# Kernel optimization log

Hardware: AMD Instinct MI355X
Metric: run time of the kernel (lower is better)

The kernel has to match this reference:

```python
import jax, jax.numpy as jnp
import numpy as np

EMBED_DIM = 768
NUM_HEADS = 8
HEAD_DIM = EMBED_DIM // NUM_HEADS
WINDOW_HALF = (17 - 1) // 2          # window_size=17 -> 8
GAP = 3 + 1                          # dilation_gap=3 -> stride 4
OVERLAP = WINDOW_HALF * GAP          # 32
N_LINES = 8192


def setup_inputs() -> dict:
    key = jax.random.key(0)
    k1, k2, k3, k4, k5 = jax.random.split(key, 5)
    D = EMBED_DIM
    return {
        "main": jax.random.normal(k1, (N_LINES, D), dtype=jnp.float32),
        "begin": jax.random.normal(k2, (OVERLAP, D), dtype=jnp.float32),
        "end": jax.random.normal(k3, (OVERLAP, D), dtype=jnp.float32),
        "in_proj_w": jax.random.normal(k4, (3 * D, D), dtype=jnp.float32) * 0.02,
        "in_proj_b": jnp.zeros((3 * D,), dtype=jnp.float32),
        "out_proj_w": jax.random.normal(k5, (D, D), dtype=jnp.float32) * 0.02,
        "out_proj_b": jnp.zeros((D,), dtype=jnp.float32),
    }


def reference(main, begin, end, in_proj_w, in_proj_b, out_proj_w, out_proj_b):
    N, D = main.shape
    H, hd = NUM_HEADS, HEAD_DIM
    # combined buffer [begin | main | end]; the per-token shifted concatenations
    # in the torch loop are equivalent to a strided gather into this buffer.
    combined = jnp.concatenate([begin, main, end], axis=0)  # [N + 2*OVERLAP, D]
    offsets = jnp.concatenate([
        jnp.arange(-OVERLAP, 0, GAP),
        jnp.arange(GAP, OVERLAP + GAP, GAP),
    ])  # [2*WINDOW_HALF] = [16]
    idx = jnp.arange(N)[:, None] + OVERLAP + offsets[None, :]  # [N, W]
    keys = combined[idx]  # [N, W, D] dilated window keys (= values)

    wq, wk, wv = in_proj_w[:D], in_proj_w[D:2 * D], in_proj_w[2 * D:]
    bq, bk, bv = in_proj_b[:D], in_proj_b[D:2 * D], in_proj_b[2 * D:]

    q = (main @ wq.T + bq).reshape(N, H, hd) * (hd ** -0.5)   # [N,H,hd]
    k = (keys @ wk.T + bk).reshape(N, -1, H, hd)              # [N,W,H,hd]
    v = (keys @ wv.T + bv).reshape(N, -1, H, hd)              # [N,W,H,hd]

    scores = jnp.einsum('nhd,nwhd->nhw', q, k)                # [N,H,W]
    attn = jax.nn.softmax(scores, axis=-1)
    ctx = jnp.einsum('nhw,nwhd->nhd', attn, v).reshape(N, D)
    attn_out = ctx @ out_proj_w.T + out_proj_b                # [N,D]
    return jnp.concatenate([main, attn_out], axis=-1)         # [N,2D]
```

## Files before the change

kernel.cpp:

```cpp
#include <hip/hip_runtime.h>
#include <math.h>

#define D 768
#define NQKV 2304
#define NH 8
#define HD 96
#define NW 16
#define OVL 32
#define NLINES 8192
#define NCOMB 8256
#define MPAD 8320
#define CH 64
#define SCALE_Q 0.1020620726159657f
#define COMB_BLOCKS 6240

typedef int i32x8 __attribute__((ext_vector_type(8)));
typedef float f32x4 __attribute__((ext_vector_type(4)));
typedef float f32x2 __attribute__((ext_vector_type(2)));

__device__ __forceinline__ unsigned int pk_fp8x4(float a, float b, float c, float d) {
    int u = __builtin_amdgcn_cvt_pk_fp8_f32(a, b, 0, false);
    u = __builtin_amdgcn_cvt_pk_fp8_f32(c, d, u, true);
    return (unsigned int)u;
}
__device__ __forceinline__ unsigned char f2fp8(float v) {
    return (unsigned char)(__builtin_amdgcn_cvt_pk_fp8_f32(v, v, 0, false) & 0xFF);
}
template <bool HI>
__device__ __forceinline__ f32x2 upk(unsigned int u) {
    return __builtin_amdgcn_cvt_pk_f32_fp8((int)u, HI);
}
__device__ __forceinline__ float dot4f8(unsigned int a, unsigned int b) {
    const f32x2 al = upk<false>(a), ah = upk<true>(a);
    const f32x2 bl = upk<false>(b), bh = upk<true>(b);
    return al.x * bl.x + al.y * bl.y + ah.x * bh.x + ah.y * bh.y;
}

__device__ __forceinline__ void stage16(const void* g, void* l) {
    __builtin_amdgcn_global_load_lds(
        (const __attribute__((address_space(1))) unsigned int*)g,
        (__attribute__((address_space(3))) unsigned int*)l, 16, 0, 0);
}

__device__ __forceinline__ void stage_sw(const unsigned char* gbase, unsigned char* lds, int ch) {
    const int row = ch >> 3;
    const int half = ch & 1;
    const int o = (((ch >> 1) & 3) - row) & 3;
    stage16(gbase + (size_t)row * D + o * 32 + half * 16, lds + ch * 16);
}

__device__ __forceinline__ int xcd_swz(int lin, int nwg) {
    const int q = nwg >> 3, r = nwg & 7;
    const int x = lin & 7, i = lin >> 3;
    return (x < r ? x * (q + 1) : r * (q + 1) + (x - r) * q) + i;
}

__global__ __launch_bounds__(256) void convert_all(const float* __restrict__ main_,
                                                   const float* __restrict__ begin_,
                                                   const float* __restrict__ end_,
                                                   const float* __restrict__ in_w,
                                                   const float* __restrict__ in_b,
                                                   const float* __restrict__ out_w,
                                                   unsigned int* __restrict__ comb_dst,
                                                   unsigned int* __restrict__ w_dst,
                                                   float* __restrict__ bias_s,
                                                   float* __restrict__ out) {
    const int bid = blockIdx.x;
    if (bid < COMB_BLOCKS) {
        const int i = bid * 256 + threadIdx.x;
        const int row = i / 192, c4 = i % 192;
        float4 v = make_float4(0.f, 0.f, 0.f, 0.f);
        if (row < NCOMB) {
            const float* src = (row < OVL) ? begin_ + (size_t)row * D
                             : (row < OVL + NLINES) ? main_ + (size_t)(row - OVL) * D
                                                    : end_ + (size_t)(row - OVL - NLINES) * D;
            v = *(const float4*)(src + c4 * 4);
            if (row >= OVL && row < OVL + NLINES)
                *(float4*)(out + (size_t)(row - OVL) * (2 * D) + c4 * 4) = v;
        }
        comb_dst[(size_t)row * 192 + c4] = pk_fp8x4(v.x, v.y, v.z, v.w);
    } else {
        const int j = (bid - COMB_BLOCKS) * 256 + threadIdx.x;
        const int f0 = j * 4;
        const bool is_out = f0 >= 3 * D * D;
        const float4 v = is_out ? *(const float4*)(out_w + (f0 - 3 * D * D))
                                : *(const float4*)(in_w + f0);
        const float s = 16.0f * ((f0 < D * D) ? SCALE_Q : 1.0f);
        w_dst[j] = pk_fp8x4(v.x * s, v.y * s, v.z * s, v.w * s);
        if (bid == COMB_BLOCKS) {
            for (int b = threadIdx.x; b < NQKV; b += 256)
                bias_s[b] = in_b[b] * (b < D ? SCALE_Q : 1.0f);
        }
    }
}

__global__ __launch_bounds__(256) void qkv_gemm(const unsigned char* __restrict__ comb,
                                                const unsigned char* __restrict__ w_f8,
                                                const float* __restrict__ bias_s,
                                                unsigned char* __restrict__ Qb,
                                                unsigned char* __restrict__ Kb,
                                                unsigned char* __restrict__ Vb) {
    __shared__ __align__(16) unsigned char As[2][128 * 128];
    __shared__ __align__(16) unsigned char Bs[2][128 * 128];
    const int lin = blockIdx.y * 18 + blockIdx.x;
    const int s = xcd_swz(lin, 18 * 65);
    const int bx = s % 18;
    const int m0 = (s / 18) * 128;
    const int n0 = bx * 128;
    const int tid = threadIdx.x;
    const int lane = tid & 63;
    const int wave = tid >> 6;
    const int wm = (wave & 1) * 64, wn = (wave >> 1) * 64;
    const int q = lane >> 4, l15 = lane & 15;
    const int swq = (q + l15) & 3;

#pragma unroll
    for (int it = 0; it < 4; it++) {
        const int ch = tid + it * 256;
        stage_sw(comb + (size_t)m0 * D, As[0], ch);
        stage_sw(w_f8 + (size_t)n0 * D, Bs[0], ch);
    }
    __syncthreads();

    f32x4 acc[4][4] = {};
    int cur = 0;
    for (int k0 = 0; k0 < D; k0 += 128) {
        if (k0 + 128 < D) {
#pragma unroll
            for (int it = 0; it < 4; it++) {
                const int ch = tid + it * 256;
                stage_sw(comb + (size_t)m0 * D + k0 + 128, As[cur ^ 1], ch);
                stage_sw(w_f8 + (size_t)n0 * D + k0 + 128, Bs[cur ^ 1], ch);
            }
        }
        i32x8 af[4], bfr[4];
#pragma unroll
        for (int i = 0; i < 4; i++)
            af[i] = *(const i32x8*)(As[cur] + (wm + i * 16 + l15) * 128 + swq * 32);
#pragma unroll
        for (int j = 0; j < 4; j++)
            bfr[j] = *(const i32x8*)(Bs[cur] + (wn + j * 16 + l15) * 128 + swq * 32);
#pragma unroll
        for (int i = 0; i < 4; i++)
#pragma unroll
            for (int j = 0; j < 4; j++)
                acc[i][j] = __builtin_amdgcn_mfma_scale_f32_16x16x128_f8f6f4(
                    af[i], bfr[j], acc[i][j], 0, 0, 0, 127, 0, 123);
        __syncthreads();
        cur ^= 1;
    }

    unsigned char* Cb = (bx < 6) ? Qb : (bx < 12 ? Kb : Vb);
    const int nloc = (bx % 6) * 128;
#pragma unroll
    for (int i = 0; i < 4; i++)
#pragma unroll
        for (int j = 0; j < 4; j++)
#pragma unroll
            for (int r = 0; r < 4; r++) {
                const int row = m0 + wm + i * 16 + q * 4 + r;
                const int col = wn + j * 16 + l15;
                Cb[(size_t)row * D + nloc + col] = f2fp8(acc[i][j][r] + bias_s[bx * 128 + col]);
            }
}

__global__ __launch_bounds__(256) void out_gemm(const unsigned char* __restrict__ ctx,
                                                const unsigned char* __restrict__ w,
                                                const float* __restrict__ bias,
                                                float* __restrict__ out) {
    __shared__ __align__(16) unsigned char As[2][64 * 128];
    __shared__ __align__(16) unsigned char Bs[2][128 * 128];
    const int lin = blockIdx.y * 6 + blockIdx.x;
    const int s = xcd_swz(lin, 6 * 128);
    const int m0 = (s / 6) * 64;
    const int n0 = (s % 6) * 128;
    const int tid = threadIdx.x;
    const int lane = tid & 63;
    const int wave = tid >> 6;
    const int wn = wave * 32;
    const int q = lane >> 4, l15 = lane & 15;
    const int swq = (q + l15) & 3;

#pragma unroll
    for (int it = 0; it < 2; it++)
        stage_sw(ctx + (size_t)m0 * D, As[0], tid + it * 256);
#pragma unroll
    for (int it = 0; it < 4; it++)
        stage_sw(w + (size_t)n0 * D, Bs[0], tid + it * 256);
    __syncthreads();

    f32x4 acc[4][2] = {};
    int cur = 0;
    for (int k0 = 0; k0 < D; k0 += 128) {
        if (k0 + 128 < D) {
#pragma unroll
            for (int it = 0; it < 2; it++)
                stage_sw(ctx + (size_t)m0 * D + k0 + 128, As[cur ^ 1], tid + it * 256);
#pragma unroll
            for (int it = 0; it < 4; it++)
                stage_sw(w + (size_t)n0 * D + k0 + 128, Bs[cur ^ 1], tid + it * 256);
        }
        i32x8 af[4], bfr[2];
#pragma unroll
        for (int i = 0; i < 4; i++)
            af[i] = *(const i32x8*)(As[cur] + (i * 16 + l15) * 128 + swq * 32);
#pragma unroll
        for (int j = 0; j < 2; j++)
            bfr[j] = *(const i32x8*)(Bs[cur] + (wn + j * 16 + l15) * 128 + swq * 32);
#pragma unroll
        for (int i = 0; i < 4; i++)
#pragma unroll
            for (int j = 0; j < 2; j++)
                acc[i][j] = __builtin_amdgcn_mfma_scale_f32_16x16x128_f8f6f4(
                    af[i], bfr[j], acc[i][j], 0, 0, 0, 127, 0, 123);
        __syncthreads();
        cur ^= 1;
    }

#pragma unroll
    for (int i = 0; i < 4; i++)
#pragma unroll
        for (int j = 0; j < 2; j++)
#pragma unroll
            for (int r = 0; r < 4; r++) {
                const int row = m0 + i * 16 + q * 4 + r;
                const int col = n0 + wn + j * 16 + l15;
                out[(size_t)row * (2 * D) + D + col] = acc[i][j][r] + bias[col];
            }
}

__global__ __launch_bounds__(256) void attn_kernel(const unsigned char* __restrict__ Q,
                                                   const unsigned char* __restrict__ K,
                                                   const unsigned char* __restrict__ V,
                                                   unsigned char* __restrict__ ctx) {
    const int lin = blockIdx.y * 128 + blockIdx.x;
    const int s = xcd_swz(lin, 128 * 8);
    const int n0 = (s % 128) * CH;
    const int h = s / 128;
    const int tid = threadIdx.x;

    __shared__ __align__(16) unsigned char sK[128 * 128];
    __shared__ __align__(16) unsigned char sV[128 * 128];
    __shared__ float sS[CH][17];

    const int l = tid & 63;
    const int wg = tid >> 6;

#pragma unroll
    for (int it = 0; it < 3; it++) {
        const int idx = tid + it * 256;
        const int row = idx / 6, c = idx % 6;
        const int slot = (c + row) & 7;
        *(uint4*)(sK + row * 128 + slot * 16) =
            *(const uint4*)(K + (size_t)(n0 + row) * D + h * HD + c * 16);
        *(uint4*)(sV + row * 128 + slot * 16) =
            *(const uint4*)(V + (size_t)(n0 + row) * D + h * HD + c * 16);
    }
    uint4 qreg[6];
#pragma unroll
    for (int c = 0; c < 6; c++)
        qreg[c] = *(const uint4*)(Q + (size_t)(n0 + l) * D + h * HD + c * 16);
    __syncthreads();

#pragma unroll
    for (int wi = 0; wi < 4; wi++) {
        const int w = wg * 4 + wi;
        const int lrow = l + 4 * w + (w >= 8 ? 4 : 0);
        float sc = 0.f;
#pragma unroll
        for (int c = 0; c < 6; c++) {
            const uint4 ka = *(const uint4*)(sK + lrow * 128 + ((c + lrow) & 7) * 16);
            sc += dot4f8(qreg[c].x, ka.x) + dot4f8(qreg[c].y, ka.y) +
                  dot4f8(qreg[c].z, ka.z) + dot4f8(qreg[c].w, ka.w);
        }
        sS[l][w] = sc;
    }
    __syncthreads();

    if (tid < CH) {
        float mx = -1e30f;
#pragma unroll
        for (int i = 0; i < NW; i++) mx = fmaxf(mx, sS[tid][i]);
        float e[NW], sum = 0.f;
#pragma unroll
        for (int i = 0; i < NW; i++) {
            e[i] = __expf(sS[tid][i] - mx);
            sum += e[i];
        }
        const float inv = 1.f / sum;
#pragma unroll
        for (int i = 0; i < NW; i++) sS[tid][i] = e[i] * inv;
    }
    __syncthreads();

    float p[NW];
#pragma unroll
    for (int i = 0; i < NW; i++) p[i] = sS[l][i];
    float acc[24] = {};
#pragma unroll
    for (int i = 0; i < NW; i++) {
        const int lrow = l + 4 * i + (i >= 8 ? 4 : 0);
        const unsigned char* vrow = sV + lrow * 128;
        const float pw = p[i];
#pragma unroll
        for (int c = 0; c < 3; c++) {
            const int off = wg * 24 + c * 8;
            const uint2 vv =
                *(const uint2*)(vrow + (((off >> 4) + lrow) & 7) * 16 + (off & 15));
            const f32x2 a0 = upk<false>(vv.x), a1 = upk<true>(vv.x);
            const f32x2 a2 = upk<false>(vv.y), a3 = upk<true>(vv.y);
            acc[c * 8 + 0] += pw * a0.x;
            acc[c * 8 + 1] += pw * a0.y;
            acc[c * 8 + 2] += pw * a1.x;
            acc[c * 8 + 3] += pw * a1.y;
            acc[c * 8 + 4] += pw * a2.x;
            acc[c * 8 + 5] += pw * a2.y;
            acc[c * 8 + 6] += pw * a3.x;
            acc[c * 8 + 7] += pw * a3.y;
        }
    }
    unsigned char* op = ctx + (size_t)(n0 + l) * D + h * HD + wg * 24;
#pragma unroll
    for (int c = 0; c < 3; c++) {
        const unsigned int u0 =
            pk_fp8x4(acc[c * 8 + 0], acc[c * 8 + 1], acc[c * 8 + 2], acc[c * 8 + 3]);
        const unsigned int u1 =
            pk_fp8x4(acc[c * 8 + 4], acc[c * 8 + 5], acc[c * 8 + 6], acc[c * 8 + 7]);
        *(uint2*)(op + c * 8) = make_uint2(u0, u1);
    }
}

extern "C" void kernel_launch(void* const* d_in, const int* in_sizes, int n_in,
                              void* d_out, int out_size, void* d_ws, size_t ws_size,
                              hipStream_t stream) {
    const float* main_ = (const float*)d_in[0];
    const float* begin_ = (const float*)d_in[1];
    const float* end_ = (const float*)d_in[2];
    const float* in_w = (const float*)d_in[3];
    const float* in_b = (const float*)d_in[4];
    const float* out_w = (const float*)d_in[5];
    const float* out_b = (const float*)d_in[6];
    float* out = (float*)d_out;

    unsigned char* comb_f8 = (unsigned char*)d_ws;
    unsigned char* w_f8 = comb_f8 + (size_t)MPAD * D;
    unsigned char* Qb = w_f8 + (size_t)4 * D * D;
    unsigned char* Kb = Qb + (size_t)MPAD * D;
    unsigned char* Vb = Kb + (size_t)MPAD * D;
    unsigned char* ctx_f8 = Vb + (size_t)MPAD * D;
    float* bias_s = (float*)(ctx_f8 + (size_t)NLINES * D);

    convert_all<<<COMB_BLOCKS + 4 * D * D / 1024, 256, 0, stream>>>(
        main_, begin_, end_, in_w, in_b, out_w, (unsigned int*)comb_f8,
        (unsigned int*)w_f8, bias_s, out);
    qkv_gemm<<<dim3(18, 65), 256, 0, stream>>>(comb_f8, w_f8, bias_s, Qb, Kb, Vb);
    attn_kernel<<<dim3(128, NH), 256, 0, stream>>>(Qb + (size_t)OVL * D, Kb, Vb, ctx_f8);
    out_gemm<<<dim3(6, 128), 256, 0, stream>>>(ctx_f8, w_f8 + (size_t)3 * D * D,
                                               out_b, out);
}
```

Measured before the change: 162.1 us.

## Fuse all four stages into one persistent cooperative kernel with grid syncs

Merges the convert, QKV GEMM, attention and output GEMM kernels into a single persistent cooperative kernel. Blocks loop over virtual tiles, share one 64KB LDS pool, and are separated by grid.sync between stages. This is meant to remove kernel launch gaps and tail effects between the four launches. The costs are lower occupancy from the 64KB LDS pool, grid-wide barrier overhead, and a persistent tile loop in place of hardware scheduling. The separate kernels remain as a fallback if the cooperative launch fails.

After: 300.7 us. 1.85x slower.

```diff
diff --git a/kernel.cpp b/kernel.cpp
--- a/kernel.cpp
+++ b/kernel.cpp
@@ -1,5 +1,8 @@
 #include <hip/hip_runtime.h>
+#include <hip/hip_cooperative_groups.h>
 #include <math.h>
+
+namespace cg = cooperative_groups;
 
 #define D 768
 #define NQKV 2304
@@ -13,6 +16,10 @@
 #define CH 64
 #define SCALE_Q 0.1020620726159657f
 #define COMB_BLOCKS 6240
+#define CONV_BLOCKS (COMB_BLOCKS + 4 * D * D / 1024)
+#define QKV_TILES (18 * 65)
+#define ATTN_TILES (128 * 8)
+#define OUT_TILES (6 * 128)
 
 typedef int i32x8 __attribute__((ext_vector_type(8)));
 typedef float f32x4 __attribute__((ext_vector_type(4)));
@@ -55,19 +62,20 @@
     return (x < r ? x * (q + 1) : r * (q + 1) + (x - r) * q) + i;
 }
 
-__global__ __launch_bounds__(256) void convert_all(const float* __restrict__ main_,
-                                                   const float* __restrict__ begin_,
-                                                   const float* __restrict__ end_,
-                                                   const float* __restrict__ in_w,
-                                                   const float* __restrict__ in_b,
-                                                   const float* __restrict__ out_w,
-                                                   unsigned int* __restrict__ comb_dst,
-                                                   unsigned int* __restrict__ w_dst,
-                                                   float* __restrict__ bias_s,
-                                                   float* __restrict__ out) {
-    const int bid = blockIdx.x;
-    if (bid < COMB_BLOCKS) {
-        const int i = bid * 256 + threadIdx.x;
+
+__device__ __forceinline__ void conv_body(int vb, int tid,
+                                          const float* __restrict__ main_,
+                                          const float* __restrict__ begin_,
+                                          const float* __restrict__ end_,
+                                          const float* __restrict__ in_w,
+                                          const float* __restrict__ in_b,
+                                          const float* __restrict__ out_w,
+                                          unsigned int* __restrict__ comb_dst,
+                                          unsigned int* __restrict__ w_dst,
+                                          float* __restrict__ bias_s,
+                                          float* __restrict__ out) {
+    if (vb < COMB_BLOCKS) {
+        const int i = vb * 256 + tid;
         const int row = i / 192, c4 = i % 192;
         float4 v = make_float4(0.f, 0.f, 0.f, 0.f);
         if (row < NCOMB) {
@@ -80,34 +88,32 @@
         }
         comb_dst[(size_t)row * 192 + c4] = pk_fp8x4(v.x, v.y, v.z, v.w);
     } else {
-        const int j = (bid - COMB_BLOCKS) * 256 + threadIdx.x;
+        const int j = (vb - COMB_BLOCKS) * 256 + tid;
         const int f0 = j * 4;
         const bool is_out = f0 >= 3 * D * D;
         const float4 v = is_out ? *(const float4*)(out_w + (f0 - 3 * D * D))
                                 : *(const float4*)(in_w + f0);
         const float s = 16.0f * ((f0 < D * D) ? SCALE_Q : 1.0f);
         w_dst[j] = pk_fp8x4(v.x * s, v.y * s, v.z * s, v.w * s);
-        if (bid == COMB_BLOCKS) {
-            for (int b = threadIdx.x; b < NQKV; b += 256)
+        if (vb == COMB_BLOCKS) {
+            for (int b = tid; b < NQKV; b += 256)
                 bias_s[b] = in_b[b] * (b < D ? SCALE_Q : 1.0f);
         }
     }
 }
 
-__global__ __launch_bounds__(256) void qkv_gemm(const unsigned char* __restrict__ comb,
-                                                const unsigned char* __restrict__ w_f8,
-                                                const float* __restrict__ bias_s,
-                                                unsigned char* __restrict__ Qb,
-                                                unsigned char* __restrict__ Kb,
-                                                unsigned char* __restrict__ Vb) {
-    __shared__ __align__(16) unsigned char As[2][128 * 128];
-    __shared__ __align__(16) unsigned char Bs[2][128 * 128];
-    const int lin = blockIdx.y * 18 + blockIdx.x;
-    const int s = xcd_swz(lin, 18 * 65);
+__device__ __forceinline__ void qkv_body(int s, int tid, unsigned char* pool,
+                                         const unsigned char* __restrict__ comb,
+                                         const unsigned char* __restrict__ w_f8,
+                                         const float* __restrict__ bias_s,
+                                         unsigned char* __restrict__ Qb,
+                                         unsigned char* __restrict__ Kb,
+                                         unsigned char* __restrict__ Vb) {
+    unsigned char* Abuf[2] = {pool, pool + 16384};
+    unsigned char* Bbuf[2] = {pool + 32768, pool + 49152};
     const int bx = s % 18;
     const int m0 = (s / 18) * 128;
     const int n0 = bx * 128;
-    const int tid = threadIdx.x;
     const int lane = tid & 63;
     const int wave = tid >> 6;
     const int wm = (wave & 1) * 64, wn = (wave >> 1) * 64;
@@ -117,8 +123,8 @@
 #pragma unroll
     for (int it = 0; it < 4; it++) {
         const int ch = tid + it * 256;
-        stage_sw(comb + (size_t)m0 * D, As[0], ch);
-        stage_sw(w_f8 + (size_t)n0 * D, Bs[0], ch);
+        stage_sw(comb + (size_t)m0 * D, Abuf[0], ch);
+        stage_sw(w_f8 + (size_t)n0 * D, Bbuf[0], ch);
     }
     __syncthreads();
 
@@ -129,17 +135,17 @@
 #pragma unroll
             for (int it = 0; it < 4; it++) {
                 const int ch = tid + it * 256;
-                stage_sw(comb + (size_t)m0 * D + k0 + 128, As[cur ^ 1], ch);
-                stage_sw(w_f8 + (size_t)n0 * D + k0 + 128, Bs[cur ^ 1], ch);
+                stage_sw(comb + (size_t)m0 * D + k0 + 128, Abuf[cur ^ 1], ch);
+                stage_sw(w_f8 + (size_t)n0 * D + k0 + 128, Bbuf[cur ^ 1], ch);
             }
         }
         i32x8 af[4], bfr[4];
 #pragma unroll
         for (int i = 0; i < 4; i++)
-            af[i] = *(const i32x8*)(As[cur] + (wm + i * 16 + l15) * 128 + swq * 32);
+            af[i] = *(const i32x8*)(Abuf[cur] + (wm + i * 16 + l15) * 128 + swq * 32);
 #pragma unroll
         for (int j = 0; j < 4; j++)
-            bfr[j] = *(const i32x8*)(Bs[cur] + (wn + j * 16 + l15) * 128 + swq * 32);
+            bfr[j] = *(const i32x8*)(Bbuf[cur] + (wn + j * 16 + l15) * 128 + swq * 32);
 #pragma unroll
         for (int i = 0; i < 4; i++)
 #pragma unroll
@@ -164,85 +170,16 @@
             }
 }
 
-__global__ __launch_bounds__(256) void out_gemm(const unsigned char* __restrict__ ctx,
-                                                const unsigned char* __restrict__ w,
-                                                const float* __restrict__ bias,
-                                                float* __restrict__ out) {
-    __shared__ __align__(16) unsigned char As[2][64 * 128];
-    __shared__ __align__(16) unsigned char Bs[2][128 * 128];
-    const int lin = blockIdx.y * 6 + blockIdx.x;
-    const int s = xcd_swz(lin, 6 * 128);
-    const int m0 = (s / 6) * 64;
-    const int n0 = (s % 6) * 128;
-    const int tid = threadIdx.x;
-    const int lane = tid & 63;
-    const int wave = tid >> 6;
-    const int wn = wave * 32;
-    const int q = lane >> 4, l15 = lane & 15;
-    const int swq = (q + l15) & 3;
-
-#pragma unroll
-    for (int it = 0; it < 2; it++)
-        stage_sw(ctx + (size_t)m0 * D, As[0], tid + it * 256);
-#pragma unroll
-    for (int it = 0; it < 4; it++)
-        stage_sw(w + (size_t)n0 * D, Bs[0], tid + it * 256);
-    __syncthreads();
-
-    f32x4 acc[4][2] = {};
-    int cur = 0;
-    for (int k0 = 0; k0 < D; k0 += 128) {
-        if (k0 + 128 < D) {
-#pragma unroll
-            for (int it = 0; it < 2; it++)
-                stage_sw(ctx + (size_t)m0 * D + k0 + 128, As[cur ^ 1], tid + it * 256);
-#pragma unroll
-            for (int it = 0; it < 4; it++)
-                stage_sw(w + (size_t)n0 * D + k0 + 128, Bs[cur ^ 1], tid + it * 256);
-        }
-        i32x8 af[4], bfr[2];
-#pragma unroll
-        for (int i = 0; i < 4; i++)
-            af[i] = *(const i32x8*)(As[cur] + (i * 16 + l15) * 128 + swq * 32);
-#pragma unroll
-        for (int j = 0; j < 2; j++)
-            bfr[j] = *(const i32x8*)(Bs[cur] + (wn + j * 16 + l15) * 128 + swq * 32);
-#pragma unroll
-        for (int i = 0; i < 4; i++)
-#pragma unroll
-            for (int j = 0; j < 2; j++)
-                acc[i][j] = __builtin_amdgcn_mfma_scale_f32_16x16x128_f8f6f4(
-                    af[i], bfr[j], acc[i][j], 0, 0, 0, 127, 0, 123);
-        __syncthreads();
-        cur ^= 1;
-    }
-
-#pragma unroll
-    for (int i = 0; i < 4; i++)
-#pragma unroll
-        for (int j = 0; j < 2; j++)
-#pragma unroll
-            for (int r = 0; r < 4; r++) {
-                const int row = m0 + i * 16 + q * 4 + r;
-                const int col = n0 + wn + j * 16 + l15;
-                out[(size_t)row * (2 * D) + D + col] = acc[i][j][r] + bias[col];
-            }
-}
-
-__global__ __launch_bounds__(256) void attn_kernel(const unsigned char* __restrict__ Q,
-                                                   const unsigned char* __restrict__ K,
-                                                   const unsigned char* __restrict__ V,
-                                                   unsigned char* __restrict__ ctx) {
-    const int lin = blockIdx.y * 128 + blockIdx.x;
-    const int s = xcd_swz(lin, 128 * 8);
+__device__ __forceinline__ void attn_body(int s, int tid, unsigned char* pool,
+                                          const unsigned char* __restrict__ Q,
+                                          const unsigned char* __restrict__ K,
+                                          const unsigned char* __restrict__ V,
+                                          unsigned char* __restrict__ ctx) {
+    unsigned char* sK = pool;
+    unsigned char* sV = pool + 16384;
+    float* sSf = (float*)(pool + 32768);
     const int n0 = (s % 128) * CH;
     const int h = s / 128;
-    const int tid = threadIdx.x;
-
-    __shared__ __align__(16) unsigned char sK[128 * 128];
-    __shared__ __align__(16) unsigned char sV[128 * 128];
-    __shared__ float sS[CH][17];
-
     const int l = tid & 63;
     const int wg = tid >> 6;
 
@@ -273,29 +210,29 @@
             sc += dot4f8(qreg[c].x, ka.x) + dot4f8(qreg[c].y, ka.y) +
                   dot4f8(qreg[c].z, ka.z) + dot4f8(qreg[c].w, ka.w);
         }
-        sS[l][w] = sc;
+        sSf[l * 17 + w] = sc;
     }
     __syncthreads();
 
     if (tid < CH) {
         float mx = -1e30f;
 #pragma unroll
-        for (int i = 0; i < NW; i++) mx = fmaxf(mx, sS[tid][i]);
+        for (int i = 0; i < NW; i++) mx = fmaxf(mx, sSf[tid * 17 + i]);
         float e[NW], sum = 0.f;
 #pragma unroll
         for (int i = 0; i < NW; i++) {
-            e[i] = __expf(sS[tid][i] - mx);
+            e[i] = __expf(sSf[tid * 17 + i] - mx);
             sum += e[i];
         }
         const float inv = 1.f / sum;
 #pragma unroll
-        for (int i = 0; i < NW; i++) sS[tid][i] = e[i] * inv;
+        for (int i = 0; i < NW; i++) sSf[tid * 17 + i] = e[i] * inv;
     }
     __syncthreads();
 
     float p[NW];
 #pragma unroll
-    for (int i = 0; i < NW; i++) p[i] = sS[l][i];
+    for (int i = 0; i < NW; i++) p[i] = sSf[l * 17 + i];
     float acc[24] = {};
 #pragma unroll
     for (int i = 0; i < NW; i++) {
@@ -328,6 +265,146 @@
             pk_fp8x4(acc[c * 8 + 4], acc[c * 8 + 5], acc[c * 8 + 6], acc[c * 8 + 7]);
         *(uint2*)(op + c * 8) = make_uint2(u0, u1);
     }
+    __syncthreads();
+}
+
+__device__ __forceinline__ void out_body(int s, int tid, unsigned char* pool,
+                                         const unsigned char* __restrict__ ctx,
+                                         const unsigned char* __restrict__ w,
+                                         const float* __restrict__ bias,
+                                         float* __restrict__ out) {
+    unsigned char* Abuf[2] = {pool, pool + 8192};
+    unsigned char* Bbuf[2] = {pool + 16384, pool + 32768};
+    const int m0 = (s / 6) * 64;
+    const int n0 = (s % 6) * 128;
+    const int lane = tid & 63;
+    const int wave = tid >> 6;
+    const int wn = wave * 32;
+    const int q = lane >> 4, l15 = lane & 15;
+    const int swq = (q + l15) & 3;
+
+#pragma unroll
+    for (int it = 0; it < 2; it++)
+        stage_sw(ctx + (size_t)m0 * D, Abuf[0], tid + it * 256);
+#pragma unroll
+    for (int it = 0; it < 4; it++)
+        stage_sw(w + (size_t)n0 * D, Bbuf[0], tid + it * 256);
+    __syncthreads();
+
+    f32x4 acc[4][2] = {};
+    int cur = 0;
+    for (int k0 = 0; k0 < D; k0 += 128) {
+        if (k0 + 128 < D) {
+#pragma unroll
+            for (int it = 0; it < 2; it++)
+                stage_sw(ctx + (size_t)m0 * D + k0 + 128, Abuf[cur ^ 1], tid + it * 256);
+#pragma unroll
+            for (int it = 0; it < 4; it++)
+                stage_sw(w + (size_t)n0 * D + k0 + 128, Bbuf[cur ^ 1], tid + it * 256);
+        }
+        i32x8 af[4], bfr[2];
+#pragma unroll
+        for (int i = 0; i < 4; i++)
+            af[i] = *(const i32x8*)(Abuf[cur] + (i * 16 + l15) * 128 + swq * 32);
+#pragma unroll
+        for (int j = 0; j < 2; j++)
+            bfr[j] = *(const i32x8*)(Bbuf[cur] + (wn + j * 16 + l15) * 128 + swq * 32);
+#pragma unroll
+        for (int i = 0; i < 4; i++)
+#pragma unroll
+            for (int j = 0; j < 2; j++)
+                acc[i][j] = __builtin_amdgcn_mfma_scale_f32_16x16x128_f8f6f4(
+                    af[i], bfr[j], acc[i][j], 0, 0, 0, 127, 0, 123);
+        __syncthreads();
+        cur ^= 1;
+    }
+
+#pragma unroll
+    for (int i = 0; i < 4; i++)
+#pragma unroll
+        for (int j = 0; j < 2; j++)
+#pragma unroll
+            for (int r = 0; r < 4; r++) {
+                const int row = m0 + i * 16 + q * 4 + r;
+                const int col = n0 + wn + j * 16 + l15;
+                out[(size_t)row * (2 * D) + D + col] = acc[i][j][r] + bias[col];
+            }
+}
+
+__global__ __launch_bounds__(256, 2) void mega(const float* __restrict__ main_,
+                                               const float* __restrict__ begin_,
+                                               const float* __restrict__ end_,
+                                               const float* __restrict__ in_w,
+                                               const float* __restrict__ in_b,
+                                               const float* __restrict__ out_w,
+                                               const float* __restrict__ out_b,
+                                               unsigned char* __restrict__ comb_f8,
+                                               unsigned char* __restrict__ w_f8,
+                                               float* __restrict__ bias_s,
+                                               unsigned char* __restrict__ Qb,
+                                               unsigned char* __restrict__ Kb,
+                                               unsigned char* __restrict__ Vb,
+                                               unsigned char* __restrict__ ctx_f8,
+                                               float* __restrict__ out) {
+    __shared__ __align__(16) unsigned char pool[65536];
+    cg::grid_group grid = cg::this_grid();
+    const int tid = threadIdx.x;
+    const int bid = blockIdx.x;
+    const int nb = gridDim.x;
+
+    for (int vb = bid; vb < CONV_BLOCKS; vb += nb)
+        conv_body(vb, tid, main_, begin_, end_, in_w, in_b, out_w,
+                  (unsigned int*)comb_f8, (unsigned int*)w_f8, bias_s, out);
+    grid.sync();
+    for (int vb = bid; vb < QKV_TILES; vb += nb)
+        qkv_body(xcd_swz(vb, QKV_TILES), tid, pool, comb_f8, w_f8, bias_s, Qb, Kb, Vb);
+    grid.sync();
+    for (int vb = bid; vb < ATTN_TILES; vb += nb)
+        attn_body(xcd_swz(vb, ATTN_TILES), tid, pool, Qb + (size_t)OVL * D, Kb, Vb, ctx_f8);
+    grid.sync();
+    for (int vb = bid; vb < OUT_TILES; vb += nb)
+        out_body(xcd_swz(vb, OUT_TILES), tid, pool, ctx_f8, w_f8 + (size_t)3 * D * D,
+                 out_b, out);
+}
+
+__global__ __launch_bounds__(256) void convert_k(const float* __restrict__ main_,
+                                                 const float* __restrict__ begin_,
+                                                 const float* __restrict__ end_,
+                                                 const float* __restrict__ in_w,
+                                                 const float* __restrict__ in_b,
+                                                 const float* __restrict__ out_w,
+                                                 unsigned int* __restrict__ comb_dst,
+                                                 unsigned int* __restrict__ w_dst,
+                                                 float* __restrict__ bias_s,
+                                                 float* __restrict__ out) {
+    conv_body(blockIdx.x, threadIdx.x, main_, begin_, end_, in_w, in_b, out_w,
+              comb_dst, w_dst, bias_s, out);
+}
+__global__ __launch_bounds__(256) void qkv_k(const unsigned char* __restrict__ comb,
+                                             const unsigned char* __restrict__ w_f8,
+                                             const float* __restrict__ bias_s,
+                                             unsigned char* __restrict__ Qb,
+                                             unsigned char* __restrict__ Kb,
+                                             unsigned char* __restrict__ Vb) {
+    __shared__ __align__(16) unsigned char pool[65536];
+    qkv_body(xcd_swz(blockIdx.y * 18 + blockIdx.x, QKV_TILES), threadIdx.x, pool,
+             comb, w_f8, bias_s, Qb, Kb, Vb);
+}
+__global__ __launch_bounds__(256) void attn_k(const unsigned char* __restrict__ Q,
+                                              const unsigned char* __restrict__ K,
+                                              const unsigned char* __restrict__ V,
+                                              unsigned char* __restrict__ ctx) {
+    __shared__ __align__(16) unsigned char pool[36864];
+    attn_body(xcd_swz(blockIdx.y * 128 + blockIdx.x, ATTN_TILES), threadIdx.x, pool,
+              Q, K, V, ctx);
+}
+__global__ __launch_bounds__(256) void out_k(const unsigned char* __restrict__ ctx,
+                                             const unsigned char* __restrict__ w,
+                                             const float* __restrict__ bias,
+                                             float* __restrict__ out) {
+    __shared__ __align__(16) unsigned char pool[49152];
+    out_body(xcd_swz(blockIdx.y * 6 + blockIdx.x, OUT_TILES), threadIdx.x, pool,
+             ctx, w, bias, out);
 }
 
 extern "C" void kernel_launch(void* const* d_in, const int* in_sizes, int n_in,
@@ -350,11 +427,27 @@
     unsigned char* ctx_f8 = Vb + (size_t)MPAD * D;
     float* bias_s = (float*)(ctx_f8 + (size_t)NLINES * D);
 
-    convert_all<<<COMB_BLOCKS + 4 * D * D / 1024, 256, 0, stream>>>(
-        main_, begin_, end_, in_w, in_b, out_w, (unsigned int*)comb_f8,
-        (unsigned int*)w_f8, bias_s, out);
-    qkv_gemm<<<dim3(18, 65), 256, 0, stream>>>(comb_f8, w_f8, bias_s, Qb, Kb, Vb);
-    attn_kernel<<<dim3(128, NH), 256, 0, stream>>>(Qb + (size_t)OVL * D, Kb, Vb, ctx_f8);
-    out_gemm<<<dim3(6, 128), 256, 0, stream>>>(ctx_f8, w_f8 + (size_t)3 * D * D,
-                                               out_b, out);
-}
+    static int maxb = -1;
+    if (maxb < 0) {
+        if (hipOccupancyMaxActiveBlocksPerMultiprocessor(&maxb, (const void*)mega, 256, 0) !=
+                hipSuccess || maxb < 1)
+            maxb = 1;
+        if (maxb > 4) maxb = 4;
+    }
+    const int grid = maxb * 256;
+
+    void* args[] = {(void*)&main_, (void*)&begin_, (void*)&end_, (void*)&in_w,
+                    (void*)&in_b, (void*)&out_w, (void*)&out_b, (void*)&comb_f8,
+                    (void*)&w_f8, (void*)&bias_s, (void*)&Qb, (void*)&Kb,
+                    (void*)&Vb, (void*)&ctx_f8, (void*)&out};
+    const hipError_t err = hipLaunchCooperativeKernel(
+        (const void*)mega, dim3(grid), dim3(256), args, 0, stream);
+    if (err != hipSuccess) {
+        convert_k<<<CONV_BLOCKS, 256, 0, stream>>>(main_, begin_, end_, in_w, in_b, out_w,
+                                                   (unsigned int*)comb_f8,
+                                                   (unsigned int*)w_f8, bias_s, out);
+        qkv_k<<<dim3(18, 65), 256, 0, stream>>>(comb_f8, w_f8, bias_s, Qb, Kb, Vb);
+        attn_k<<<dim3(128, NH), 256, 0, stream>>>(Qb + (size_t)OVL * D, Kb, Vb, ctx_f8);
+        out_k<<<dim3(6, 128), 256, 0, stream>>>(ctx_f8, w_f8 + (size_t)3 * D * D, out_b, out);
+    }
+}
```
